# Kernel tuning notes

Hardware: AMD Instinct MI355X
Metric: run time of the kernel (lower is better)

The kernel has to match this reference:

```python
import jax, jax.numpy as jnp
import numpy as np

N, NU, R, NX, NY = 16384, 2, 256, 8, 2


def setup_inputs() -> dict:
    key = jax.random.key(0)
    ks = jax.random.split(key, 10)
    A = jax.random.normal(ks[0], (NX, NX), dtype=jnp.float32)
    # scale A to be stable (spectral radius < 1) so the 16k-step recurrence is well-behaved
    rho = jnp.max(jnp.abs(jnp.linalg.eigvals(A.astype(jnp.float32)))).real
    A = (A * (0.95 / rho)).astype(jnp.float32)
    return {
        "u": jax.random.normal(ks[1], (N, NU, R), dtype=jnp.float32),
        "x0": jax.random.normal(ks[2], (NX, R), dtype=jnp.float32),
        "A": A,
        "B_u": jax.random.normal(ks[3], (NX, NU), dtype=jnp.float32),
        "C_y": jax.random.normal(ks[4], (NY, NX), dtype=jnp.float32),
        "D_yu": jax.random.normal(ks[5], (NY, NU), dtype=jnp.float32),
        "u_mean": jax.random.normal(ks[6], (NU,), dtype=jnp.float32),
        "u_std": jax.random.uniform(ks[7], (NU,), dtype=jnp.float32, minval=0.5, maxval=1.5),
        "y_mean": jax.random.normal(ks[8], (NY,), dtype=jnp.float32),
        "y_std": jax.random.uniform(ks[9], (NY,), dtype=jnp.float32, minval=0.5, maxval=1.5),
    }


def reference(u, x0, A, B_u, C_y, D_yu, u_mean, u_std, y_mean, y_std):
    # normalize input as in _simulate_core
    un = (u - u_mean.reshape(1, -1, 1)) / u_std.reshape(1, -1, 1)  # (N, nu, R)

    def step(x, uk):
        # x: (nx, R), uk: (nu, R)
        y = C_y @ x + D_yu @ uk      # (ny, R)
        x_next = A @ x + B_u @ uk    # (nx, R)
        return x_next, (y, x)

    _, (Y, X) = jax.lax.scan(step, x0, un)  # Y: (N, ny, R), X: (N, nx, R)

    # denormalize output
    y = Y * y_std.reshape(1, -1, 1) + y_mean.reshape(1, -1, 1)
    return y, X
```

## Files before the change

### kernel.cpp

```cpp
#include <hip/hip_runtime.h>


#define NSTEPS 16384
#define NUI 2
#define RB 256
#define NXS 8
#define NYO 2
#define LF 32
#define NC1 (NSTEPS / LF)
#define NC2 (NC1 / 4)

__global__ void pow_k(const float* __restrict__ A, float* __restrict__ A32,
                      float* __restrict__ A64, float* __restrict__ A96,
                      float* __restrict__ A128) {
    __shared__ float M[64], T32[64];
    const int t = threadIdx.x;
    const int i = t >> 3, j = t & 7;
    M[t] = A[t];
    __syncthreads();
    for (int it = 0; it < 5; ++it) {
        float acc = 0.f;
        #pragma unroll
        for (int k = 0; k < 8; ++k) acc += M[i * 8 + k] * M[k * 8 + j];
        __syncthreads();
        M[t] = acc;
        __syncthreads();
    }
    T32[t] = M[t];
    A32[t] = M[t];
    {
        float acc = 0.f;
        #pragma unroll
        for (int k = 0; k < 8; ++k) acc += M[i * 8 + k] * M[k * 8 + j];
        __syncthreads();
        M[t] = acc;
        __syncthreads();
    }
    A64[t] = M[t];
    float a96 = 0.f, a128 = 0.f;
    #pragma unroll
    for (int k = 0; k < 8; ++k) {
        a96  += M[i * 8 + k] * T32[k * 8 + j];
        a128 += M[i * 8 + k] * M[k * 8 + j];
    }
    A96[t] = a96;
    A128[t] = a128;
}

__global__ __launch_bounds__(RB) void phase1_k(
    const float* __restrict__ u, const float* __restrict__ A,
    const float* __restrict__ Bu, const float* __restrict__ um,
    const float* __restrict__ us, float* __restrict__ d32) {
    const int c = blockIdx.x;
    const int r = threadIdx.x;
    float a[NXS][NXS];
    #pragma unroll
    for (int i = 0; i < NXS; ++i)
        #pragma unroll
        for (int j = 0; j < NXS; ++j) a[i][j] = A[i * NXS + j];
    float b0[NXS], b1[NXS];
    #pragma unroll
    for (int i = 0; i < NXS; ++i) { b0[i] = Bu[i * NUI]; b1[i] = Bu[i * NUI + 1]; }
    const float um0 = um[0], um1 = um[1];
    const float is0 = 1.0f / us[0], is1 = 1.0f / us[1];
    float t[NXS];
    #pragma unroll
    for (int i = 0; i < NXS; ++i) t[i] = 0.f;
    const float* up = u + (size_t)c * LF * NUI * RB + r;
    #pragma unroll 4
    for (int j = 0; j < LF; ++j) {
        const float u0 = (up[0]  - um0) * is0;
        const float u1 = (up[RB] - um1) * is1;
        up += NUI * RB;
        float nt[NXS];
        #pragma unroll
        for (int i = 0; i < NXS; ++i) {
            float acc = fmaf(b0[i], u0, b1[i] * u1);
            #pragma unroll
            for (int k = 0; k < NXS; ++k) acc = fmaf(a[i][k], t[k], acc);
            nt[i] = acc;
        }
        #pragma unroll
        for (int i = 0; i < NXS; ++i) t[i] = nt[i];
    }
    float* dp = d32 + (size_t)c * NXS * RB + r;
    #pragma unroll
    for (int i = 0; i < NXS; ++i) dp[i * RB] = t[i];
}

__global__ __launch_bounds__(RB) void combine4_k(
    const float* __restrict__ d32, const float* __restrict__ A32,
    const float* __restrict__ A64, const float* __restrict__ A96,
    float* __restrict__ d128) {
    const int m = blockIdx.x;
    const int r = threadIdx.x;
    float m32[NXS][NXS], m64[NXS][NXS], m96[NXS][NXS];
    #pragma unroll
    for (int i = 0; i < NXS; ++i)
        #pragma unroll
        for (int j = 0; j < NXS; ++j) {
            m32[i][j] = A32[i * NXS + j];
            m64[i][j] = A64[i * NXS + j];
            m96[i][j] = A96[i * NXS + j];
        }
    const float* p = d32 + (size_t)(4 * m) * NXS * RB + r;
    float x0[NXS], x1[NXS], x2[NXS], x3[NXS];
    #pragma unroll
    for (int i = 0; i < NXS; ++i) {
        x0[i] = p[i * RB];
        x1[i] = p[(size_t)NXS * RB + i * RB];
        x2[i] = p[(size_t)2 * NXS * RB + i * RB];
        x3[i] = p[(size_t)3 * NXS * RB + i * RB];
    }
    float* o = d128 + (size_t)m * NXS * RB + r;
    #pragma unroll
    for (int i = 0; i < NXS; ++i) {
        float acc = x3[i];
        #pragma unroll
        for (int k = 0; k < NXS; ++k) {
            acc = fmaf(m96[i][k], x0[k], acc);
            acc = fmaf(m64[i][k], x1[k], acc);
            acc = fmaf(m32[i][k], x2[k], acc);
        }
        o[i * RB] = acc;
    }
}

__global__ __launch_bounds__(64) void phase2_k(
    const float* __restrict__ x0, const float* __restrict__ A128,
    const float* __restrict__ d128, float* __restrict__ s128) {
    const int r = blockIdx.x * 64 + threadIdx.x;
    float m[NXS][NXS];
    #pragma unroll
    for (int i = 0; i < NXS; ++i)
        #pragma unroll
        for (int j = 0; j < NXS; ++j) m[i][j] = A128[i * NXS + j];
    float s[NXS];
    #pragma unroll
    for (int i = 0; i < NXS; ++i) s[i] = x0[i * RB + r];
    float P[8][NXS];
    #pragma unroll
    for (int sl = 0; sl < 8; ++sl) {
        const float* dp = d128 + (size_t)sl * NXS * RB + r;
        #pragma unroll
        for (int i = 0; i < NXS; ++i) P[sl][i] = dp[i * RB];
    }
    for (int c = 0; c < NC2; c += 8) {
        #pragma unroll
        for (int sl = 0; sl < 8; ++sl) {
            const int cc = c + sl;
            float* sp = s128 + (size_t)cc * NXS * RB + r;
            #pragma unroll
            for (int i = 0; i < NXS; ++i) sp[i * RB] = s[i];
            float ns[NXS];
            #pragma unroll
            for (int i = 0; i < NXS; ++i) {
                float acc = P[sl][i];
                #pragma unroll
                for (int k = 0; k < NXS; ++k) acc = fmaf(m[i][k], s[k], acc);
                ns[i] = acc;
            }
            if (cc + 8 < NC2) {
                const float* dp = d128 + (size_t)(cc + 8) * NXS * RB + r;
                #pragma unroll
                for (int i = 0; i < NXS; ++i) P[sl][i] = dp[i * RB];
            }
            #pragma unroll
            for (int i = 0; i < NXS; ++i) s[i] = ns[i];
        }
    }
}

__global__ __launch_bounds__(RB) void phase3_k(
    const float* __restrict__ u, const float* __restrict__ s128,
    const float* __restrict__ d32, const float* __restrict__ A32,
    const float* __restrict__ A, const float* __restrict__ Bu,
    const float* __restrict__ Cy, const float* __restrict__ Dyu,
    const float* __restrict__ um, const float* __restrict__ us,
    const float* __restrict__ ym, const float* __restrict__ ys,
    float* __restrict__ Y, float* __restrict__ X) {
    const int c = blockIdx.x;
    const int r = threadIdx.x;
    const int m = c >> 2;
    const int p = c & 3;
    float a[NXS][NXS];
    #pragma unroll
    for (int i = 0; i < NXS; ++i)
        #pragma unroll
        for (int j = 0; j < NXS; ++j) a[i][j] = A[i * NXS + j];
    float b0[NXS], b1[NXS], c0[NXS], c1[NXS];
    #pragma unroll
    for (int i = 0; i < NXS; ++i) { b0[i] = Bu[i * NUI]; b1[i] = Bu[i * NUI + 1]; }
    #pragma unroll
    for (int k = 0; k < NXS; ++k) { c0[k] = Cy[k]; c1[k] = Cy[NXS + k]; }
    const float d00 = Dyu[0], d01 = Dyu[1], d10 = Dyu[2], d11 = Dyu[3];
    const float um0 = um[0], um1 = um[1];
    const float is0 = 1.0f / us[0], is1 = 1.0f / us[1];
    const float ym0 = ym[0], ym1 = ym[1], ys0 = ys[0], ys1 = ys[1];

    float t[NXS];
    {
        const float* sp = s128 + (size_t)m * NXS * RB + r;
        #pragma unroll
        for (int i = 0; i < NXS; ++i) t[i] = sp[i * RB];
    }
    if (p) {
        float a32[NXS][NXS];
        #pragma unroll
        for (int i = 0; i < NXS; ++i)
            #pragma unroll
            for (int j = 0; j < NXS; ++j) a32[i][j] = A32[i * NXS + j];
        for (int q = 0; q < p; ++q) {
            const float* dp = d32 + (size_t)(4 * m + q) * NXS * RB + r;
            float nt[NXS];
            #pragma unroll
            for (int i = 0; i < NXS; ++i) {
                float acc = dp[i * RB];
                #pragma unroll
                for (int k = 0; k < NXS; ++k) acc = fmaf(a32[i][k], t[k], acc);
                nt[i] = acc;
            }
            #pragma unroll
            for (int i = 0; i < NXS; ++i) t[i] = nt[i];
        }
    }

    const float* up = u + (size_t)c * LF * NUI * RB + r;
    float* Xp = X + (size_t)c * LF * NXS * RB + r;
    float* Yp = Y + (size_t)c * LF * NYO * RB + r;
    #pragma unroll 4
    for (int j = 0; j < LF; ++j) {
        const float u0 = (up[0]  - um0) * is0;
        const float u1 = (up[RB] - um1) * is1;
        up += NUI * RB;
        #pragma unroll
        for (int i = 0; i < NXS; ++i)
            __builtin_nontemporal_store(t[i], Xp + i * RB);
        Xp += NXS * RB;
        float y0 = fmaf(d00, u0, d01 * u1);
        float y1 = fmaf(d10, u0, d11 * u1);
        #pragma unroll
        for (int k = 0; k < NXS; ++k) {
            y0 = fmaf(c0[k], t[k], y0);
            y1 = fmaf(c1[k], t[k], y1);
        }
        __builtin_nontemporal_store(fmaf(y0, ys0, ym0), Yp);
        __builtin_nontemporal_store(fmaf(y1, ys1, ym1), Yp + RB);
        Yp += NYO * RB;
        float nt[NXS];
        #pragma unroll
        for (int i = 0; i < NXS; ++i) {
            float acc = fmaf(b0[i], u0, b1[i] * u1);
            #pragma unroll
            for (int k = 0; k < NXS; ++k) acc = fmaf(a[i][k], t[k], acc);
            nt[i] = acc;
        }
        #pragma unroll
        for (int i = 0; i < NXS; ++i) t[i] = nt[i];
    }
}

extern "C" void kernel_launch(void* const* d_in, const int* in_sizes, int n_in,
                              void* d_out, int out_size, void* d_ws, size_t ws_size,
                              hipStream_t stream) {
    const float* u   = (const float*)d_in[0];
    const float* x0  = (const float*)d_in[1];
    const float* A   = (const float*)d_in[2];
    const float* Bu  = (const float*)d_in[3];
    const float* Cy  = (const float*)d_in[4];
    const float* Dyu = (const float*)d_in[5];
    const float* um  = (const float*)d_in[6];
    const float* us  = (const float*)d_in[7];
    const float* ym  = (const float*)d_in[8];
    const float* ys  = (const float*)d_in[9];

    float* Y = (float*)d_out;
    float* X = Y + (size_t)NSTEPS * NYO * RB;

    float* ws   = (float*)d_ws;
    float* A32  = ws;
    float* A64  = ws + 64;
    float* A96  = ws + 128;
    float* A128 = ws + 192;
    float* d32  = ws + 256;
    float* d128 = d32 + (size_t)NC1 * NXS * RB;
    float* s128 = d128 + (size_t)NC2 * NXS * RB;

    pow_k<<<1, 64, 0, stream>>>(A, A32, A64, A96, A128);
    phase1_k<<<NC1, RB, 0, stream>>>(u, A, Bu, um, us, d32);
    combine4_k<<<NC2, RB, 0, stream>>>(d32, A32, A64, A96, d128);
    phase2_k<<<4, 64, 0, stream>>>(x0, A128, d128, s128);
    phase3_k<<<NC1, RB, 0, stream>>>(u, s128, d32, A32, A, Bu, Cy, Dyu,
                                     um, us, ym, ys, Y, X);
}
```

Baseline: 254.6 us.

## Fuse chunked scan phases into one cooperative kernel with grid syncs

Replaces the five-kernel chunked linear-recurrence pipeline with one cooperative kernel. It uses grid-wide syncs between the local-scan, super-chunk combine, serial prefix and output phases. Normalized inputs stay in shared memory across phases so they are not reloaded, and X/Y writes use nontemporal stores. The serial prefix now runs over 64 super-chunks of 256 steps using A^256 instead of 128-step chunks. The goal is to remove launch overhead and input re-reads. In exchange, all 512 blocks must be co-resident, and a fallback to the old path covers the case where the cooperative launch fails.

```diff
diff --git a/kernel.cpp b/kernel.cpp
--- a/kernel.cpp
+++ b/kernel.cpp
@@ -1,4 +1,7 @@
 #include <hip/hip_runtime.h>
+#include <hip/hip_cooperative_groups.h>
+
+namespace cg = cooperative_groups;
 
 
 #define NSTEPS 16384
@@ -9,6 +12,247 @@
 #define LF 32
 #define NC1 (NSTEPS / LF)
 #define NC2 (NC1 / 4)
+#define NSUP 8
+#define NC2B (NC1 / NSUP)
+
+__global__ __launch_bounds__(RB, 2) void fused_k(
+    const float* __restrict__ u, const float* __restrict__ x0,
+    const float* __restrict__ A, const float* __restrict__ Bu,
+    const float* __restrict__ Cy, const float* __restrict__ Dyu,
+    const float* __restrict__ um, const float* __restrict__ us,
+    const float* __restrict__ ym, const float* __restrict__ ys,
+    float* __restrict__ Y, float* __restrict__ X,
+    float* __restrict__ d32, float* __restrict__ d256,
+    float* __restrict__ s256) {
+    __shared__ float uL[LF][NUI][RB];
+    __shared__ float Ms[64];
+    __shared__ float A32s[64];
+    __shared__ float A256s[64];
+
+    const int c = blockIdx.x;
+    const int t = threadIdx.x;
+    const int r = t;
+    cg::grid_group grid = cg::this_grid();
+
+    if (t < 64) Ms[t] = A[t];
+    __syncthreads();
+    {
+        const int pi = t >> 3, pj = t & 7;
+        for (int it = 0; it < 8; ++it) {
+            float acc = 0.f;
+            if (t < 64) {
+                #pragma unroll
+                for (int k = 0; k < 8; ++k) acc += Ms[pi * 8 + k] * Ms[k * 8 + pj];
+            }
+            __syncthreads();
+            if (t < 64) {
+                Ms[t] = acc;
+                if (it == 4) A32s[t] = acc;
+            }
+            __syncthreads();
+        }
+        if (t < 64) A256s[t] = Ms[t];
+        __syncthreads();
+    }
+
+    float a[NXS][NXS];
+    #pragma unroll
+    for (int i = 0; i < NXS; ++i)
+        #pragma unroll
+        for (int j = 0; j < NXS; ++j) a[i][j] = A[i * NXS + j];
+    float b0[NXS], b1[NXS];
+    #pragma unroll
+    for (int i = 0; i < NXS; ++i) { b0[i] = Bu[i * NUI]; b1[i] = Bu[i * NUI + 1]; }
+    const float um0 = um[0], um1 = um[1];
+    const float is0 = 1.0f / us[0], is1 = 1.0f / us[1];
+    {
+        float tv[NXS];
+        #pragma unroll
+        for (int i = 0; i < NXS; ++i) tv[i] = 0.f;
+        const float* up = u + (size_t)c * LF * NUI * RB + r;
+        #pragma unroll 4
+        for (int j = 0; j < LF; ++j) {
+            const float u0 = (up[0]  - um0) * is0;
+            const float u1 = (up[RB] - um1) * is1;
+            up += NUI * RB;
+            uL[j][0][r] = u0;
+            uL[j][1][r] = u1;
+            float nt[NXS];
+            #pragma unroll
+            for (int i = 0; i < NXS; ++i) {
+                float acc = fmaf(b0[i], u0, b1[i] * u1);
+                #pragma unroll
+                for (int k = 0; k < NXS; ++k) acc = fmaf(a[i][k], tv[k], acc);
+                nt[i] = acc;
+            }
+            #pragma unroll
+            for (int i = 0; i < NXS; ++i) tv[i] = nt[i];
+        }
+        float* dp = d32 + (size_t)c * NXS * RB + r;
+        #pragma unroll
+        for (int i = 0; i < NXS; ++i) dp[i * RB] = tv[i];
+    }
+    __threadfence();
+    grid.sync();
+
+    if (c < NC2B) {
+        float a32[NXS][NXS];
+        #pragma unroll
+        for (int i = 0; i < NXS; ++i)
+            #pragma unroll
+            for (int j = 0; j < NXS; ++j) a32[i][j] = A32s[i * 8 + j];
+        float xq[NSUP][NXS];
+        #pragma unroll
+        for (int q = 0; q < NSUP; ++q) {
+            const float* dq = d32 + (size_t)(NSUP * c + q) * NXS * RB + r;
+            #pragma unroll
+            for (int i = 0; i < NXS; ++i) xq[q][i] = dq[i * RB];
+        }
+        float s[NXS];
+        #pragma unroll
+        for (int i = 0; i < NXS; ++i) s[i] = xq[0][i];
+        #pragma unroll
+        for (int q = 1; q < NSUP; ++q) {
+            float nt[NXS];
+            #pragma unroll
+            for (int i = 0; i < NXS; ++i) {
+                float acc = xq[q][i];
+                #pragma unroll
+                for (int k = 0; k < NXS; ++k) acc = fmaf(a32[i][k], s[k], acc);
+                nt[i] = acc;
+            }
+            #pragma unroll
+            for (int i = 0; i < NXS; ++i) s[i] = nt[i];
+        }
+        float* o = d256 + (size_t)c * NXS * RB + r;
+        #pragma unroll
+        for (int i = 0; i < NXS; ++i) o[i * RB] = s[i];
+    }
+    __threadfence();
+    grid.sync();
+
+    if (c == 0) {
+        float mm[NXS][NXS];
+        #pragma unroll
+        for (int i = 0; i < NXS; ++i)
+            #pragma unroll
+            for (int j = 0; j < NXS; ++j) mm[i][j] = A256s[i * 8 + j];
+        float s[NXS];
+        #pragma unroll
+        for (int i = 0; i < NXS; ++i) s[i] = x0[i * RB + r];
+        float P[8][NXS];
+        #pragma unroll
+        for (int sl = 0; sl < 8; ++sl) {
+            const float* dp = d256 + (size_t)sl * NXS * RB + r;
+            #pragma unroll
+            for (int i = 0; i < NXS; ++i) P[sl][i] = dp[i * RB];
+        }
+        for (int cc = 0; cc < NC2B; cc += 8) {
+            #pragma unroll
+            for (int sl = 0; sl < 8; ++sl) {
+                const int q = cc + sl;
+                float* sp = s256 + (size_t)q * NXS * RB + r;
+                #pragma unroll
+                for (int i = 0; i < NXS; ++i) sp[i * RB] = s[i];
+                float ns[NXS];
+                #pragma unroll
+                for (int i = 0; i < NXS; ++i) {
+                    float acc = P[sl][i];
+                    #pragma unroll
+                    for (int k = 0; k < NXS; ++k) acc = fmaf(mm[i][k], s[k], acc);
+                    ns[i] = acc;
+                }
+                if (q + 8 < NC2B) {
+                    const float* dp = d256 + (size_t)(q + 8) * NXS * RB + r;
+                    #pragma unroll
+                    for (int i = 0; i < NXS; ++i) P[sl][i] = dp[i * RB];
+                }
+                #pragma unroll
+                for (int i = 0; i < NXS; ++i) s[i] = ns[i];
+            }
+        }
+    }
+    __threadfence();
+    grid.sync();
+
+    {
+        const int m = c >> 3;
+        const int p = c & 7;
+        float tv[NXS];
+        {
+            const float* sp = s256 + (size_t)m * NXS * RB + r;
+            #pragma unroll
+            for (int i = 0; i < NXS; ++i) tv[i] = sp[i * RB];
+        }
+        if (p) {
+            float a32[NXS][NXS];
+            #pragma unroll
+            for (int i = 0; i < NXS; ++i)
+                #pragma unroll
+                for (int j = 0; j < NXS; ++j) a32[i][j] = A32s[i * 8 + j];
+            float Pq[NSUP - 1][NXS];
+            #pragma unroll
+            for (int q = 0; q < NSUP - 1; ++q) {
+                if (q < p) {
+                    const float* dp = d32 + (size_t)(NSUP * m + q) * NXS * RB + r;
+                    #pragma unroll
+                    for (int i = 0; i < NXS; ++i) Pq[q][i] = dp[i * RB];
+                }
+            }
+            #pragma unroll
+            for (int q = 0; q < NSUP - 1; ++q) {
+                if (q < p) {
+                    float nt[NXS];
+                    #pragma unroll
+                    for (int i = 0; i < NXS; ++i) {
+                        float acc = Pq[q][i];
+                        #pragma unroll
+                        for (int k = 0; k < NXS; ++k) acc = fmaf(a32[i][k], tv[k], acc);
+                        nt[i] = acc;
+                    }
+                    #pragma unroll
+                    for (int i = 0; i < NXS; ++i) tv[i] = nt[i];
+                }
+            }
+        }
+        float c0[NXS], c1[NXS];
+        #pragma unroll
+        for (int k = 0; k < NXS; ++k) { c0[k] = Cy[k]; c1[k] = Cy[NXS + k]; }
+        const float d00 = Dyu[0], d01 = Dyu[1], d10 = Dyu[2], d11 = Dyu[3];
+        const float ym0 = ym[0], ym1 = ym[1], ys0 = ys[0], ys1 = ys[1];
+        float* Xp = X + (size_t)c * LF * NXS * RB + r;
+        float* Yp = Y + (size_t)c * LF * NYO * RB + r;
+        #pragma unroll 4
+        for (int j = 0; j < LF; ++j) {
+            const float u0 = uL[j][0][r];
+            const float u1 = uL[j][1][r];
+            #pragma unroll
+            for (int i = 0; i < NXS; ++i)
+                __builtin_nontemporal_store(tv[i], Xp + i * RB);
+            Xp += NXS * RB;
+            float y0 = fmaf(d00, u0, d01 * u1);
+            float y1 = fmaf(d10, u0, d11 * u1);
+            #pragma unroll
+            for (int k = 0; k < NXS; ++k) {
+                y0 = fmaf(c0[k], tv[k], y0);
+                y1 = fmaf(c1[k], tv[k], y1);
+            }
+            __builtin_nontemporal_store(fmaf(y0, ys0, ym0), Yp);
+            __builtin_nontemporal_store(fmaf(y1, ys1, ym1), Yp + RB);
+            Yp += NYO * RB;
+            float nt[NXS];
+            #pragma unroll
+            for (int i = 0; i < NXS; ++i) {
+                float acc = fmaf(b0[i], u0, b1[i] * u1);
+                #pragma unroll
+                for (int k = 0; k < NXS; ++k) acc = fmaf(a[i][k], tv[k], acc);
+                nt[i] = acc;
+            }
+            #pragma unroll
+            for (int i = 0; i < NXS; ++i) tv[i] = nt[i];
+        }
+    }
+}
 
 __global__ void pow_k(const float* __restrict__ A, float* __restrict__ A32,
                       float* __restrict__ A64, float* __restrict__ A96,
@@ -278,18 +522,27 @@
     float* X = Y + (size_t)NSTEPS * NYO * RB;
 
     float* ws   = (float*)d_ws;
-    float* A32  = ws;
-    float* A64  = ws + 64;
-    float* A96  = ws + 128;
-    float* A128 = ws + 192;
-    float* d32  = ws + 256;
-    float* d128 = d32 + (size_t)NC1 * NXS * RB;
-    float* s128 = d128 + (size_t)NC2 * NXS * RB;
-
-    pow_k<<<1, 64, 0, stream>>>(A, A32, A64, A96, A128);
-    phase1_k<<<NC1, RB, 0, stream>>>(u, A, Bu, um, us, d32);
-    combine4_k<<<NC2, RB, 0, stream>>>(d32, A32, A64, A96, d128);
-    phase2_k<<<4, 64, 0, stream>>>(x0, A128, d128, s128);
-    phase3_k<<<NC1, RB, 0, stream>>>(u, s128, d32, A32, A, Bu, Cy, Dyu,
-                                     um, us, ym, ys, Y, X);
-}
+    float* d32  = ws;
+    float* dsup = d32 + (size_t)NC1 * NXS * RB;
+    float* ssup = dsup + (size_t)NC2 * NXS * RB;
+    float* Apow = ssup + (size_t)NC2 * NXS * RB;
+
+    void* args[] = { (void*)&u,  (void*)&x0, (void*)&A,   (void*)&Bu,
+                     (void*)&Cy, (void*)&Dyu,(void*)&um,  (void*)&us,
+                     (void*)&ym, (void*)&ys, (void*)&Y,   (void*)&X,
+                     (void*)&d32,(void*)&dsup,(void*)&ssup };
+    hipError_t err = hipLaunchCooperativeKernel(fused_k, dim3(NC1), dim3(RB),
+                                                args, 0, stream);
+    if (err != hipSuccess) {
+        float* A32  = Apow;
+        float* A64  = Apow + 64;
+        float* A96  = Apow + 128;
+        float* A128 = Apow + 192;
+        pow_k<<<1, 64, 0, stream>>>(A, A32, A64, A96, A128);
+        phase1_k<<<NC1, RB, 0, stream>>>(u, A, Bu, um, us, d32);
+        combine4_k<<<NC2, RB, 0, stream>>>(d32, A32, A64, A96, dsup);
+        phase2_k<<<4, 64, 0, stream>>>(x0, A128, dsup, ssup);
+        phase3_k<<<NC1, RB, 0, stream>>>(u, ssup, d32, A32, A, Bu, Cy, Dyu,
+                                         um, us, ym, ys, Y, X);
+    }
+}
```

Result: slower. 553.0 us (+117.2%).

## Remove pow kernel, recompute A powers in-kernel, widen superchunk to 256 steps

Applied to the files above, without the earlier changes.

Drops the separate matrix-power kernel, so combine, phase2 and phase3 each recompute A^32 (and A^256 in phase2) by repeated squaring in shared memory. The superchunk grows from 4 to 8 chunks, which halves the serial phase2 loop length. The combine step now uses a sequential Horner-style chain with A^32 in place of precomputed A^64/A^96. The intent is to cut one kernel launch and shorten the serial critical path. In exchange, phase3 blocks do up to 7 sequential prefix steps, and every block pays for redundant squaring and barriers.

```diff
diff --git a/kernel.cpp b/kernel.cpp
--- a/kernel.cpp
+++ b/kernel.cpp
@@ -8,44 +8,8 @@
 #define NYO 2
 #define LF 32
 #define NC1 (NSTEPS / LF)
-#define NC2 (NC1 / 4)
-
-__global__ void pow_k(const float* __restrict__ A, float* __restrict__ A32,
-                      float* __restrict__ A64, float* __restrict__ A96,
-                      float* __restrict__ A128) {
-    __shared__ float M[64], T32[64];
-    const int t = threadIdx.x;
-    const int i = t >> 3, j = t & 7;
-    M[t] = A[t];
-    __syncthreads();
-    for (int it = 0; it < 5; ++it) {
-        float acc = 0.f;
-        #pragma unroll
-        for (int k = 0; k < 8; ++k) acc += M[i * 8 + k] * M[k * 8 + j];
-        __syncthreads();
-        M[t] = acc;
-        __syncthreads();
-    }
-    T32[t] = M[t];
-    A32[t] = M[t];
-    {
-        float acc = 0.f;
-        #pragma unroll
-        for (int k = 0; k < 8; ++k) acc += M[i * 8 + k] * M[k * 8 + j];
-        __syncthreads();
-        M[t] = acc;
-        __syncthreads();
-    }
-    A64[t] = M[t];
-    float a96 = 0.f, a128 = 0.f;
-    #pragma unroll
-    for (int k = 0; k < 8; ++k) {
-        a96  += M[i * 8 + k] * T32[k * 8 + j];
-        a128 += M[i * 8 + k] * M[k * 8 + j];
-    }
-    A96[t] = a96;
-    A128[t] = a128;
-}
+#define NSUP 8
+#define NC2B (NC1 / NSUP)
 
 __global__ __launch_bounds__(RB) void phase1_k(
     const float* __restrict__ u, const float* __restrict__ A,
@@ -88,68 +52,110 @@
     for (int i = 0; i < NXS; ++i) dp[i * RB] = t[i];
 }
 
-__global__ __launch_bounds__(RB) void combine4_k(
-    const float* __restrict__ d32, const float* __restrict__ A32,
-    const float* __restrict__ A64, const float* __restrict__ A96,
-    float* __restrict__ d128) {
+__global__ __launch_bounds__(RB) void combine8_k(
+    const float* __restrict__ d32, const float* __restrict__ A,
+    float* __restrict__ d256) {
+    __shared__ float Ms[64];
+    __shared__ float A32s[64];
     const int m = blockIdx.x;
-    const int r = threadIdx.x;
-    float m32[NXS][NXS], m64[NXS][NXS], m96[NXS][NXS];
+    const int t = threadIdx.x;
+    const int r = t;
+
+    float xq[NSUP][NXS];
+    #pragma unroll
+    for (int q = 0; q < NSUP; ++q) {
+        const float* dq = d32 + (size_t)(NSUP * m + q) * NXS * RB + r;
+        #pragma unroll
+        for (int i = 0; i < NXS; ++i) xq[q][i] = dq[i * RB];
+    }
+
+    if (t < 64) Ms[t] = A[t];
+    __syncthreads();
+    {
+        const int pi = t >> 3, pj = t & 7;
+        for (int it = 0; it < 5; ++it) {
+            float acc = 0.f;
+            if (t < 64) {
+                #pragma unroll
+                for (int k = 0; k < 8; ++k) acc += Ms[pi * 8 + k] * Ms[k * 8 + pj];
+            }
+            __syncthreads();
+            if (t < 64) Ms[t] = acc;
+            __syncthreads();
+        }
+        if (t < 64) A32s[t] = Ms[t];
+        __syncthreads();
+    }
+
+    float a32[NXS][NXS];
     #pragma unroll
     for (int i = 0; i < NXS; ++i)
         #pragma unroll
-        for (int j = 0; j < NXS; ++j) {
-            m32[i][j] = A32[i * NXS + j];
-            m64[i][j] = A64[i * NXS + j];
-            m96[i][j] = A96[i * NXS + j];
-        }
-    const float* p = d32 + (size_t)(4 * m) * NXS * RB + r;
-    float x0[NXS], x1[NXS], x2[NXS], x3[NXS];
-    #pragma unroll
-    for (int i = 0; i < NXS; ++i) {
-        x0[i] = p[i * RB];
-        x1[i] = p[(size_t)NXS * RB + i * RB];
-        x2[i] = p[(size_t)2 * NXS * RB + i * RB];
-        x3[i] = p[(size_t)3 * NXS * RB + i * RB];
-    }
-    float* o = d128 + (size_t)m * NXS * RB + r;
-    #pragma unroll
-    for (int i = 0; i < NXS; ++i) {
-        float acc = x3[i];
-        #pragma unroll
-        for (int k = 0; k < NXS; ++k) {
-            acc = fmaf(m96[i][k], x0[k], acc);
-            acc = fmaf(m64[i][k], x1[k], acc);
-            acc = fmaf(m32[i][k], x2[k], acc);
-        }
-        o[i * RB] = acc;
-    }
+        for (int j = 0; j < NXS; ++j) a32[i][j] = A32s[i * 8 + j];
+
+    float s[NXS];
+    #pragma unroll
+    for (int i = 0; i < NXS; ++i) s[i] = xq[0][i];
+    #pragma unroll
+    for (int q = 1; q < NSUP; ++q) {
+        float nt[NXS];
+        #pragma unroll
+        for (int i = 0; i < NXS; ++i) {
+            float acc = xq[q][i];
+            #pragma unroll
+            for (int k = 0; k < NXS; ++k) acc = fmaf(a32[i][k], s[k], acc);
+            nt[i] = acc;
+        }
+        #pragma unroll
+        for (int i = 0; i < NXS; ++i) s[i] = nt[i];
+    }
+    float* o = d256 + (size_t)m * NXS * RB + r;
+    #pragma unroll
+    for (int i = 0; i < NXS; ++i) o[i * RB] = s[i];
 }
 
 __global__ __launch_bounds__(64) void phase2_k(
-    const float* __restrict__ x0, const float* __restrict__ A128,
-    const float* __restrict__ d128, float* __restrict__ s128) {
-    const int r = blockIdx.x * 64 + threadIdx.x;
-    float m[NXS][NXS];
-    #pragma unroll
-    for (int i = 0; i < NXS; ++i)
-        #pragma unroll
-        for (int j = 0; j < NXS; ++j) m[i][j] = A128[i * NXS + j];
+    const float* __restrict__ x0, const float* __restrict__ A,
+    const float* __restrict__ d256, float* __restrict__ s256) {
+    __shared__ float Ms[64];
+    const int t = threadIdx.x;
+    const int r = blockIdx.x * 64 + t;
+
     float s[NXS];
     #pragma unroll
     for (int i = 0; i < NXS; ++i) s[i] = x0[i * RB + r];
     float P[8][NXS];
     #pragma unroll
     for (int sl = 0; sl < 8; ++sl) {
-        const float* dp = d128 + (size_t)sl * NXS * RB + r;
+        const float* dp = d256 + (size_t)sl * NXS * RB + r;
         #pragma unroll
         for (int i = 0; i < NXS; ++i) P[sl][i] = dp[i * RB];
     }
-    for (int c = 0; c < NC2; c += 8) {
+
+    Ms[t] = A[t];
+    __syncthreads();
+    {
+        const int pi = t >> 3, pj = t & 7;
+        for (int it = 0; it < 8; ++it) {
+            float acc = 0.f;
+            #pragma unroll
+            for (int k = 0; k < 8; ++k) acc += Ms[pi * 8 + k] * Ms[k * 8 + pj];
+            __syncthreads();
+            Ms[t] = acc;
+            __syncthreads();
+        }
+    }
+    float m[NXS][NXS];
+    #pragma unroll
+    for (int i = 0; i < NXS; ++i)
+        #pragma unroll
+        for (int j = 0; j < NXS; ++j) m[i][j] = Ms[i * 8 + j];
+
+    for (int c = 0; c < NC2B; c += 8) {
         #pragma unroll
         for (int sl = 0; sl < 8; ++sl) {
             const int cc = c + sl;
-            float* sp = s128 + (size_t)cc * NXS * RB + r;
+            float* sp = s256 + (size_t)cc * NXS * RB + r;
             #pragma unroll
             for (int i = 0; i < NXS; ++i) sp[i * RB] = s[i];
             float ns[NXS];
@@ -160,8 +166,8 @@
                 for (int k = 0; k < NXS; ++k) acc = fmaf(m[i][k], s[k], acc);
                 ns[i] = acc;
             }
-            if (cc + 8 < NC2) {
-                const float* dp = d128 + (size_t)(cc + 8) * NXS * RB + r;
+            if (cc + 8 < NC2B) {
+                const float* dp = d256 + (size_t)(cc + 8) * NXS * RB + r;
                 #pragma unroll
                 for (int i = 0; i < NXS; ++i) P[sl][i] = dp[i * RB];
             }
@@ -172,17 +178,83 @@
 }
 
 __global__ __launch_bounds__(RB) void phase3_k(
-    const float* __restrict__ u, const float* __restrict__ s128,
-    const float* __restrict__ d32, const float* __restrict__ A32,
-    const float* __restrict__ A, const float* __restrict__ Bu,
-    const float* __restrict__ Cy, const float* __restrict__ Dyu,
-    const float* __restrict__ um, const float* __restrict__ us,
-    const float* __restrict__ ym, const float* __restrict__ ys,
-    float* __restrict__ Y, float* __restrict__ X) {
+    const float* __restrict__ u, const float* __restrict__ s256,
+    const float* __restrict__ d32, const float* __restrict__ A,
+    const float* __restrict__ Bu, const float* __restrict__ Cy,
+    const float* __restrict__ Dyu, const float* __restrict__ um,
+    const float* __restrict__ us, const float* __restrict__ ym,
+    const float* __restrict__ ys, float* __restrict__ Y,
+    float* __restrict__ X) {
+    __shared__ float Ms[64];
+    __shared__ float A32s[64];
     const int c = blockIdx.x;
-    const int r = threadIdx.x;
-    const int m = c >> 2;
-    const int p = c & 3;
+    const int t = threadIdx.x;
+    const int r = t;
+    const int m = c >> 3;
+    const int p = c & 7;
+
+    float tv[NXS];
+    {
+        const float* sp = s256 + (size_t)m * NXS * RB + r;
+        #pragma unroll
+        for (int i = 0; i < NXS; ++i) tv[i] = sp[i * RB];
+    }
+
+    if (t < 64) Ms[t] = A[t];
+    __syncthreads();
+    {
+        const int pi = t >> 3, pj = t & 7;
+        for (int it = 0; it < 5; ++it) {
+            float acc = 0.f;
+            if (t < 64) {
+                #pragma unroll
+                for (int k = 0; k < 8; ++k) acc += Ms[pi * 8 + k] * Ms[k * 8 + pj];
+            }
+            __syncthreads();
+            if (t < 64) Ms[t] = acc;
+            __syncthreads();
+        }
+        if (t < 64) A32s[t] = Ms[t];
+        __syncthreads();
+    }
+
+    if (p) {
+        float a32[NXS][NXS];
+        #pragma unroll
+        for (int i = 0; i < NXS; ++i)
+            #pragma unroll
+            for (int j = 0; j < NXS; ++j) a32[i][j] = A32s[i * 8 + j];
+        float Pa[NXS], Pb[NXS];
+        const float* dp0 = d32 + (size_t)(NSUP * m) * NXS * RB + r;
+        #pragma unroll
+        for (int i = 0; i < NXS; ++i) Pa[i] = dp0[i * RB];
+        #pragma unroll
+        for (int q = 0; q < NSUP - 1; ++q) {
+            if (q < p) {
+                if (q + 1 < p) {
+                    const float* dn = d32 + (size_t)(NSUP * m + q + 1) * NXS * RB + r;
+                    if (q & 1) {
+                        #pragma unroll
+                        for (int i = 0; i < NXS; ++i) Pa[i] = dn[i * RB];
+                    } else {
+                        #pragma unroll
+                        for (int i = 0; i < NXS; ++i) Pb[i] = dn[i * RB];
+                    }
+                }
+                float nt[NXS];
+                #pragma unroll
+                for (int i = 0; i < NXS; ++i) {
+                    float acc = (q & 1) ? Pb[i] : Pa[i];
+                    #pragma unroll
+                    for (int k = 0; k < NXS; ++k) acc = fmaf(a32[i][k], tv[k], acc);
+                    nt[i] = acc;
+                }
+                #pragma unroll
+                for (int i = 0; i < NXS; ++i) tv[i] = nt[i];
+            }
+        }
+    }
+
     float a[NXS][NXS];
     #pragma unroll
     for (int i = 0; i < NXS; ++i)
@@ -197,33 +269,6 @@
     const float um0 = um[0], um1 = um[1];
     const float is0 = 1.0f / us[0], is1 = 1.0f / us[1];
     const float ym0 = ym[0], ym1 = ym[1], ys0 = ys[0], ys1 = ys[1];
-
-    float t[NXS];
-    {
-        const float* sp = s128 + (size_t)m * NXS * RB + r;
-        #pragma unroll
-        for (int i = 0; i < NXS; ++i) t[i] = sp[i * RB];
-    }
-    if (p) {
-        float a32[NXS][NXS];
-        #pragma unroll
-        for (int i = 0; i < NXS; ++i)
-            #pragma unroll
-            for (int j = 0; j < NXS; ++j) a32[i][j] = A32[i * NXS + j];
-        for (int q = 0; q < p; ++q) {
-            const float* dp = d32 + (size_t)(4 * m + q) * NXS * RB + r;
-            float nt[NXS];
-            #pragma unroll
-            for (int i = 0; i < NXS; ++i) {
-                float acc = dp[i * RB];
-                #pragma unroll
-                for (int k = 0; k < NXS; ++k) acc = fmaf(a32[i][k], t[k], acc);
-                nt[i] = acc;
-            }
-            #pragma unroll
-            for (int i = 0; i < NXS; ++i) t[i] = nt[i];
-        }
-    }
 
     const float* up = u + (size_t)c * LF * NUI * RB + r;
     float* Xp = X + (size_t)c * LF * NXS * RB + r;
@@ -235,14 +280,14 @@
         up += NUI * RB;
         #pragma unroll
         for (int i = 0; i < NXS; ++i)
-            __builtin_nontemporal_store(t[i], Xp + i * RB);
+            __builtin_nontemporal_store(tv[i], Xp + i * RB);
         Xp += NXS * RB;
         float y0 = fmaf(d00, u0, d01 * u1);
         float y1 = fmaf(d10, u0, d11 * u1);
         #pragma unroll
         for (int k = 0; k < NXS; ++k) {
-            y0 = fmaf(c0[k], t[k], y0);
-            y1 = fmaf(c1[k], t[k], y1);
+            y0 = fmaf(c0[k], tv[k], y0);
+            y1 = fmaf(c1[k], tv[k], y1);
         }
         __builtin_nontemporal_store(fmaf(y0, ys0, ym0), Yp);
         __builtin_nontemporal_store(fmaf(y1, ys1, ym1), Yp + RB);
@@ -252,11 +297,11 @@
         for (int i = 0; i < NXS; ++i) {
             float acc = fmaf(b0[i], u0, b1[i] * u1);
             #pragma unroll
-            for (int k = 0; k < NXS; ++k) acc = fmaf(a[i][k], t[k], acc);
+            for (int k = 0; k < NXS; ++k) acc = fmaf(a[i][k], tv[k], acc);
             nt[i] = acc;
         }
         #pragma unroll
-        for (int i = 0; i < NXS; ++i) t[i] = nt[i];
+        for (int i = 0; i < NXS; ++i) tv[i] = nt[i];
     }
 }
 
@@ -278,18 +323,13 @@
     float* X = Y + (size_t)NSTEPS * NYO * RB;
 
     float* ws   = (float*)d_ws;
-    float* A32  = ws;
-    float* A64  = ws + 64;
-    float* A96  = ws + 128;
-    float* A128 = ws + 192;
-    float* d32  = ws + 256;
-    float* d128 = d32 + (size_t)NC1 * NXS * RB;
-    float* s128 = d128 + (size_t)NC2 * NXS * RB;
-
-    pow_k<<<1, 64, 0, stream>>>(A, A32, A64, A96, A128);
+    float* d32  = ws;
+    float* d256 = d32 + (size_t)NC1 * NXS * RB;
+    float* s256 = d256 + (size_t)NC2B * NXS * RB;
+
     phase1_k<<<NC1, RB, 0, stream>>>(u, A, Bu, um, us, d32);
-    combine4_k<<<NC2, RB, 0, stream>>>(d32, A32, A64, A96, d128);
-    phase2_k<<<4, 64, 0, stream>>>(x0, A128, d128, s128);
-    phase3_k<<<NC1, RB, 0, stream>>>(u, s128, d32, A32, A, Bu, Cy, Dyu,
+    combine8_k<<<NC2B, RB, 0, stream>>>(d32, A, d256);
+    phase2_k<<<4, 64, 0, stream>>>(x0, A, d256, s256);
+    phase3_k<<<NC1, RB, 0, stream>>>(u, s256, d32, A, Bu, Cy, Dyu,
                                      um, us, ym, ys, Y, X);
 }
```

Result: faster. 236.6 us (-7.1%).
